# Optimization experiments

Hardware: AMD Instinct MI355X
Metric: run time of the kernel (lower is better)

The kernel has to match this reference:

```python
import jax, jax.numpy as jnp
import numpy as np

N_NODES = 50000
N_EDGES = 800000
IN_FEATS = 256
N_HEADS = 4
OUT_FEATS = 32
NEG_SLOPE = 0.2


def setup_inputs() -> dict:
    key = jax.random.key(0)
    k_feat, k_src, k_dst, k_fc, k_al, k_ar, k_res = jax.random.split(key, 7)
    feat = jax.random.normal(k_feat, (N_NODES, IN_FEATS), dtype=jnp.float32)
    src = jax.random.randint(k_src, (N_EDGES,), 0, N_NODES)
    dst = jax.random.randint(k_dst, (N_EDGES,), 0, N_NODES)
    # xavier-normal-ish scales
    s_fc = (2.0 / (IN_FEATS + N_HEADS * OUT_FEATS)) ** 0.5
    W_fc = jax.random.normal(k_fc, (N_HEADS * OUT_FEATS, IN_FEATS), dtype=jnp.float32) * s_fc
    s_a = (2.0 / (1 + N_HEADS * OUT_FEATS)) ** 0.5
    attn_l = jax.random.normal(k_al, (N_HEADS, OUT_FEATS), dtype=jnp.float32) * s_a
    attn_r = jax.random.normal(k_ar, (N_HEADS, OUT_FEATS), dtype=jnp.float32) * s_a
    W_res = jax.random.normal(k_res, (N_HEADS * OUT_FEATS, IN_FEATS), dtype=jnp.float32) * s_fc
    return {"feat": feat, "src": src, "dst": dst, "W_fc": W_fc,
            "attn_l": attn_l, "attn_r": attn_r, "W_res": W_res}


def reference(feat, src, dst, W_fc, attn_l, attn_r, W_res):
    N = feat.shape[0]
    H, D = attn_l.shape
    ones_e = jnp.ones(src.shape[0], dtype=feat.dtype)

    # projection: [N, H, D]
    h = (feat @ W_fc.T).reshape(N, H, D)
    feat_dst = h  # dst features are pre-norm (torch code aliases before * norm)

    # symmetric norm on source side: out_degree^-0.5
    out_deg = jax.ops.segment_sum(ones_e, src, num_segments=N)
    feat_src = h * (jnp.clip(out_deg, 1.0) ** -0.5)[:, None, None]

    # per-node attention halves -> per-edge score, leaky relu
    el = jnp.einsum('nhd,hd->nh', feat_src, attn_l)  # [N, H]
    er = jnp.einsum('nhd,hd->nh', feat_dst, attn_r)  # [N, H]
    e = jax.nn.leaky_relu(el[src] + er[dst], NEG_SLOPE)  # [E, H]

    # edge_softmax over incoming edges of each dst node
    emax = jax.ops.segment_max(e, dst, num_segments=N)
    emax = jnp.where(jnp.isfinite(emax), emax, 0.0)  # guard empty segments
    ex = jnp.exp(e - emax[dst])
    denom = jax.ops.segment_sum(ex, dst, num_segments=N)
    a = ex / denom[dst]  # [E, H]

    # weighted scatter-sum of messages: u_mul_e + sum
    msg = feat_src[src] * a[:, :, None]  # [E, H, D]
    rst = jax.ops.segment_sum(msg, dst, num_segments=N)  # [N, H, D]

    # symmetric norm on destination side: in_degree^0.5
    in_deg = jax.ops.segment_sum(ones_e, dst, num_segments=N)
    rst = rst * jnp.sqrt(jnp.clip(in_deg, 1.0))[:, None, None]

    # residual projection
    rst = rst + (feat @ W_res.T).reshape(N, H, D)
    return rst
```

## Files before the change

### kernel.cpp

```cpp
#include <hip/hip_runtime.h>
#include <hip/hip_bf16.h>
#include <math.h>

#define HD 128
#define IN_F 256
#define NEG_SLOPE 0.2f
#define NMAX 50000
#define GGRID 256
#define CSRC 32

typedef __attribute__((ext_vector_type(8))) short short8;
typedef __attribute__((ext_vector_type(4))) float f32x4;

__device__ __forceinline__ unsigned short f2bf(float x) {
    __hip_bfloat16 b = __float2bfloat16(x);
    return *(unsigned short*)&b;
}
__device__ __forceinline__ float bf2f(unsigned short u) {
    unsigned int v = ((unsigned int)u) << 16;
    float f;
    __builtin_memcpy(&f, &v, 4);
    return f;
}
__device__ __forceinline__ short8 pack8(float4 f0, float4 f1) {
    short8 v;
    v[0] = (short)f2bf(f0.x); v[1] = (short)f2bf(f0.y);
    v[2] = (short)f2bf(f0.z); v[3] = (short)f2bf(f0.w);
    v[4] = (short)f2bf(f1.x); v[5] = (short)f2bf(f1.y);
    v[6] = (short)f2bf(f1.z); v[7] = (short)f2bf(f1.w);
    return v;
}

__global__ __launch_bounds__(256) void cvt_ew_kernel(
    const float4* __restrict__ wfc4, const float4* __restrict__ wres4,
    const float* __restrict__ wfc, const float* __restrict__ attn_l,
    const float* __restrict__ attn_r, ushort4* __restrict__ w16,
    unsigned short* __restrict__ ew16, int n4each) {
    int b = blockIdx.x;
    if (b < 4) {
        int h = b, k = threadIdx.x;
        float sl = 0.f, sr = 0.f;
#pragma unroll 8
        for (int d = 0; d < 32; d++) {
            float w = wfc[(size_t)(h * 32 + d) * IN_F + k];
            sl += attn_l[h * 32 + d] * w;
            sr += attn_r[h * 32 + d] * w;
        }
        ew16[h * IN_F + k] = f2bf(sl);
        ew16[(4 + h) * IN_F + k] = f2bf(sr);
        ew16[(8 + h) * IN_F + k] = 0;
        ew16[(12 + h) * IN_F + k] = 0;
        return;
    }
    int idx = (b - 4) * 256 + threadIdx.x;
    if (idx >= 2 * n4each) return;
    float4 f = (idx < n4each) ? wfc4[idx] : wres4[idx - n4each];
    ushort4 u;
    u.x = f2bf(f.x); u.y = f2bf(f.y); u.z = f2bf(f.z); u.w = f2bf(f.w);
    w16[idx] = u;
}

__global__ __launch_bounds__(512) void hist_kernel(const int* __restrict__ src,
                                                   const int* __restrict__ dst,
                                                   unsigned short* __restrict__ pc_src,
                                                   unsigned short* __restrict__ pc_dst,
                                                   int N, int E, int C, int chunk,
                                                   int chunk_s) {
    __shared__ unsigned int h[NMAX / 2];
    int tid = threadIdx.x;
    int nh = N >> 1;
    uint4* h4 = (uint4*)h;
    for (int i = tid; i < (nh >> 2); i += 512) h4[i] = make_uint4(0, 0, 0, 0);
    for (int i = (nh & ~3) + tid; i < nh; i += 512) h[i] = 0;
    __syncthreads();

    int b = blockIdx.x;
    bool isSrc = (b >= C);
    const int* arr = isSrc ? src : dst;
    int c = isSrc ? (b - C) : b;
    int ch = isSrc ? chunk_s : chunk;
    int e0 = c * ch, e1 = min(E, (c + 1) * ch);
    for (int e = e0 + tid; e < e1; e += 512) {
        int v = arr[e];
        atomicAdd(&h[v >> 1], 1u << ((v & 1) << 4));
    }
    __syncthreads();

    unsigned short* pc = (isSrc ? pc_src : pc_dst) + (size_t)c * N;
    uint4* pc4 = (uint4*)pc;
    for (int i = tid; i < (nh >> 2); i += 512) pc4[i] = h4[i];
    for (int i = (nh & ~3) + tid; i < nh; i += 512) ((unsigned int*)pc)[i] = h[i];
}

__global__ __launch_bounds__(256) void sum_scan1_kernel(
    const unsigned short* __restrict__ pc_src, unsigned short* __restrict__ pc_dst,
    int* __restrict__ out_cnt, int* __restrict__ deg, int* __restrict__ bsum,
    int N, int C) {
    __shared__ int wsum[4];
    int n = blockIdx.x * 256 + threadIdx.x;
    int sd = 0;
    if (n < N) {
        int ss = 0;
#pragma unroll 4
        for (int c = 0; c < CSRC; c++) ss += pc_src[(size_t)c * N + n];
        for (int c = 0; c < C; c++) {
            unsigned short v = pc_dst[(size_t)c * N + n];
            pc_dst[(size_t)c * N + n] = (unsigned short)sd;
            sd += v;
        }
        out_cnt[n] = ss;
        deg[n] = sd;
    }
    int v = (n < N) ? sd : 0;
#pragma unroll
    for (int d = 1; d < 64; d <<= 1) v += __shfl_xor(v, d);
    if ((threadIdx.x & 63) == 0) wsum[threadIdx.x >> 6] = v;
    __syncthreads();
    if (threadIdx.x == 0) bsum[blockIdx.x] = wsum[0] + wsum[1] + wsum[2] + wsum[3];
}

__global__ __launch_bounds__(256) void scan3_kernel(const int* __restrict__ deg,
                                                    const int* __restrict__ bsum,
                                                    int* __restrict__ row_start,
                                                    int N, int nb, int E) {
    __shared__ int wsum[4];
    __shared__ int sbo[256];
    int tid = threadIdx.x, lane = tid & 63, wid = tid >> 6;
    {
        int v = (tid < nb) ? bsum[tid] : 0;
        int incl = v;
#pragma unroll
        for (int d = 1; d < 64; d <<= 1) {
            int t = __shfl_up(incl, d);
            if (lane >= d) incl += t;
        }
        if (lane == 63) wsum[wid] = incl;
        __syncthreads();
        int woff = 0;
        for (int w = 0; w < wid; w++) woff += wsum[w];
        sbo[tid] = woff + incl - v;
        __syncthreads();
    }
    int boff = sbo[blockIdx.x];
    if (blockIdx.x == 0 && tid == 0) row_start[N] = E;
    __syncthreads();

    int i = blockIdx.x * 256 + tid;
    int v = (i < N) ? deg[i] : 0;
    int incl = v;
#pragma unroll
    for (int d = 1; d < 64; d <<= 1) {
        int t = __shfl_up(incl, d);
        if (lane >= d) incl += t;
    }
    if (lane == 63) wsum[wid] = incl;
    __syncthreads();
    int woff = 0;
    for (int w = 0; w < wid; w++) woff += wsum[w];
    int excl = boff + woff + incl - v;
    if (i < N) row_start[i] = excl;
}

__global__ __launch_bounds__(512) void place_kernel(const int* __restrict__ src,
                                                    const int* __restrict__ dst,
                                                    const unsigned short* __restrict__ chunkpre,
                                                    const int* __restrict__ row_start,
                                                    int* __restrict__ esrc,
                                                    int N, int E, int chunk) {
    __shared__ unsigned int cur[NMAX / 2];
    int tid = threadIdx.x;
    int nh = N >> 1;
    const unsigned short* cp = chunkpre + (size_t)blockIdx.x * N;
    const uint4* cp4 = (const uint4*)cp;
    uint4* cur4 = (uint4*)cur;
    for (int i = tid; i < (nh >> 2); i += 512) cur4[i] = cp4[i];
    for (int i = (nh & ~3) + tid; i < nh; i += 512) cur[i] = ((const unsigned int*)cp)[i];
    __syncthreads();

    int e1 = min(E, (int)(blockIdx.x + 1) * chunk);
    for (int e = blockIdx.x * chunk + tid; e < e1; e += 512) {
        int d = dst[e], s = src[e];
        int sh = (d & 1) << 4;
        unsigned int old = atomicAdd(&cur[d >> 1], 1u << sh);
        int rank = (old >> sh) & 0xffff;
        esrc[row_start[d] + rank] = s;
    }
}

__global__ __launch_bounds__(512, 1) void gemm_fused(
    const float* __restrict__ feat, const __hip_bfloat16* __restrict__ w16,
    const __hip_bfloat16* __restrict__ ew16, const int* __restrict__ out_cnt,
    unsigned short* __restrict__ h16, unsigned short* __restrict__ resid16,
    float* __restrict__ el, float* __restrict__ er, int N, int ntiles) {
    __shared__ unsigned short sB[256 * 256];
    __shared__ unsigned short sA[32 * 256];
    int tid = threadIdx.x;
    int lane = tid & 63, w = tid >> 6;
    int l15 = lane & 15, lg = lane >> 4;
    int c0 = w * 32;
    bool w0 = (w == 0);
    bool isH = (w < 4);
    int colloc = c0 & 127;

#pragma unroll
    for (int it = 0; it < 16; ++it) {
        int idx = it * 512 + tid;
        int c = idx >> 5, g = idx & 31;
        short8 v = *(const short8*)(w16 + (size_t)c * IN_F + g * 8);
        *(short8*)&sB[c * 256 + ((g ^ (c & 7)) * 8)] = v;
    }
    short8 ereg[8];
    if (w0) {
        const __hip_bfloat16* ep = ew16 + (size_t)l15 * IN_F + lg * 8;
#pragma unroll
        for (int kk = 0; kk < 8; kk++) ereg[kk] = *(const short8*)(ep + kk * 32);
    }

    int srow[2], sgc[2];
#pragma unroll
    for (int i = 0; i < 2; i++) {
        int idx = i * 512 + tid;
        srow[i] = idx >> 5;
        sgc[i] = idx & 31;
    }

    float4 fA[2][2];
    int t = blockIdx.x;
#pragma unroll
    for (int i = 0; i < 2; i++) {
        int gm = t * 32 + srow[i];
        gm = (gm < N) ? gm : (N - 1);
        const float4* fp = (const float4*)(feat + (size_t)gm * IN_F + sgc[i] * 8);
        fA[i][0] = fp[0];
        fA[i][1] = fp[1];
    }

    for (; t < ntiles; t += GGRID) {
        __syncthreads();
#pragma unroll
        for (int i = 0; i < 2; i++)
            *(short8*)&sA[srow[i] * 256 + ((sgc[i] ^ (srow[i] & 7)) * 8)] =
                pack8(fA[i][0], fA[i][1]);
        __syncthreads();

        int tn = t + GGRID;
        if (tn < ntiles) {
#pragma unroll
            for (int i = 0; i < 2; i++) {
                int gm = tn * 32 + srow[i];
                gm = (gm < N) ? gm : (N - 1);
                const float4* fp = (const float4*)(feat + (size_t)gm * IN_F + sgc[i] * 8);
                fA[i][0] = fp[0];
                fA[i][1] = fp[1];
            }
        }

        f32x4 acc[2][2], accE[2];
#pragma unroll
        for (int i = 0; i < 2; i++) {
            accE[i] = (f32x4){0.f, 0.f, 0.f, 0.f};
#pragma unroll
            for (int j = 0; j < 2; j++) acc[i][j] = (f32x4){0.f, 0.f, 0.f, 0.f};
        }
#pragma unroll
        for (int kk = 0; kk < 8; kk++) {
            short8 a[2], b[2];
#pragma unroll
            for (int mi = 0; mi < 2; mi++) {
                int row = mi * 16 + l15;
                int gs = (kk * 4 + lg) ^ (row & 7);
                a[mi] = *(const short8*)&sA[row * 256 + gs * 8];
            }
#pragma unroll
            for (int ni = 0; ni < 2; ni++) {
                int c = c0 + ni * 16 + l15;
                int gsb = (kk * 4 + lg) ^ (c & 7);
                b[ni] = *(const short8*)&sB[c * 256 + gsb * 8];
            }
#pragma unroll
            for (int mi = 0; mi < 2; mi++)
#pragma unroll
                for (int ni = 0; ni < 2; ni++)
                    acc[mi][ni] = __builtin_amdgcn_mfma_f32_16x16x32_bf16(
                        a[mi], b[ni], acc[mi][ni], 0, 0, 0);
            if (w0) {
#pragma unroll
                for (int mi = 0; mi < 2; mi++)
                    accE[mi] = __builtin_amdgcn_mfma_f32_16x16x32_bf16(
                        a[mi], ereg[kk], accE[mi], 0, 0, 0);
            }
        }

        int bm = t * 32;
#pragma unroll
        for (int mi = 0; mi < 2; mi++) {
#pragma unroll
            for (int reg = 0; reg < 4; reg++) {
                int r = bm + mi * 16 + lg * 4 + reg;
                bool valid = (r < N);
                int rr = valid ? r : 0;
                if (isH) {
                    float nrm = rsqrtf(fmaxf((float)out_cnt[rr], 1.0f));
                    if (valid) {
#pragma unroll
                        for (int ni = 0; ni < 2; ni++)
                            h16[(size_t)r * HD + colloc + ni * 16 + l15] =
                                f2bf(acc[mi][ni][reg] * nrm);
                        if (w0) {
                            float ev = accE[mi][reg];
                            if (l15 < 4) el[r * 4 + l15] = ev * nrm;
                            else if (l15 < 8) er[r * 4 + (l15 - 4)] = ev;
                        }
                    }
                } else if (valid) {
#pragma unroll
                    for (int ni = 0; ni < 2; ni++)
                        resid16[(size_t)r * HD + colloc + ni * 16 + l15] =
                            f2bf(acc[mi][ni][reg]);
                }
            }
        }
    }
}

__global__ __launch_bounds__(256) void agg_kernel(const unsigned short* __restrict__ h16,
                                                  const float* __restrict__ el,
                                                  const float* __restrict__ er,
                                                  const int* __restrict__ row_start,
                                                  const int* __restrict__ esrc,
                                                  const unsigned short* __restrict__ resid16,
                                                  float* __restrict__ out, int N) {
    int wid = threadIdx.x >> 6, lane = threadIdx.x & 63;
    int n = blockIdx.x * 4 + wid;
    if (n >= N) return;
    int es = lane >> 4;
    int l15 = lane & 15;
    int h = l15 >> 2;
    int d0 = l15 * 8;
    int beg = row_start[n], end = row_start[n + 1];
    float erh = er[n * 4 + h];
    float den = 0.f;
    float acc[8];
#pragma unroll
    for (int j = 0; j < 8; j++) acc[j] = 0.f;

    if (beg < end) {
        bool ok[4]; float ev[4]; short8 hv[4];
        auto LOAD = [&](int base, bool* okk, float* evv, short8* hvv) {
#pragma unroll
            for (int u = 0; u < 4; u++) {
                int idx = base + u * 4 + es;
                okk[u] = idx < end;
                int s = esrc[okk[u] ? idx : beg];
                evv[u] = el[s * 4 + h];
                hvv[u] = *(const short8*)(h16 + (size_t)s * HD + d0);
            }
        };
        auto COMPUTE = [&](const bool* okk, const float* evv, const short8* hvv) {
#pragma unroll
            for (int u = 0; u < 4; u++) {
                float e = evv[u] + erh;
                e = (e > 0.f) ? e : NEG_SLOPE * e;
                float ex = okk[u] ? __expf(e) : 0.f;
                den += ex;
#pragma unroll
                for (int j = 0; j < 8; j++)
                    acc[j] += ex * bf2f((unsigned short)hvv[u][j]);
            }
        };
        LOAD(beg, ok, ev, hv);
        for (int base = beg + 16; base < end; base += 16) {
            bool ok2[4]; float ev2[4]; short8 hv2[4];
            LOAD(base, ok2, ev2, hv2);
            COMPUTE(ok, ev, hv);
#pragma unroll
            for (int u = 0; u < 4; u++) { ok[u] = ok2[u]; ev[u] = ev2[u]; hv[u] = hv2[u]; }
        }
        COMPUTE(ok, ev, hv);
    }

#pragma unroll
    for (int m = 16; m < 64; m <<= 1) {
        den += __shfl_xor(den, m);
#pragma unroll
        for (int j = 0; j < 8; j++) acc[j] += __shfl_xor(acc[j], m);
    }

    if (es == 0) {
        const unsigned short* rp = resid16 + (size_t)n * HD + d0;
        short8 rv = *(const short8*)rp;
        int indeg = end - beg;
        float sc = (indeg > 0) ? sqrtf((float)indeg) / den : 0.f;
        float o[8];
#pragma unroll
        for (int j = 0; j < 8; j++)
            o[j] = sc * acc[j] + bf2f((unsigned short)rv[j]);
        float* op = out + (size_t)n * HD + d0;
        *(float4*)op = make_float4(o[0], o[1], o[2], o[3]);
        *(float4*)(op + 4) = make_float4(o[4], o[5], o[6], o[7]);
    }
}

extern "C" void kernel_launch(void* const* d_in, const int* in_sizes, int n_in,
                              void* d_out, int out_size, void* d_ws, size_t ws_size,
                              hipStream_t stream) {
    const float* feat   = (const float*)d_in[0];
    const int*   src    = (const int*)d_in[1];
    const int*   dst    = (const int*)d_in[2];
    const float* W_fc   = (const float*)d_in[3];
    const float* attn_l = (const float*)d_in[4];
    const float* attn_r = (const float*)d_in[5];
    const float* W_res  = (const float*)d_in[6];
    float* out = (float*)d_out;

    int N = in_sizes[0] / IN_F;
    int E = in_sizes[1];
    int nb = (N + 255) / 256;

    size_t off = 0;
    auto alloc = [&](size_t bytes) {
        size_t o = off;
        off = (off + bytes + 255) & ~(size_t)255;
        return o;
    };
    char* ws = (char*)d_ws;
    unsigned short* h16     = (unsigned short*)(ws + alloc((size_t)N * HD * 2));
    unsigned short* resid16 = (unsigned short*)(ws + alloc((size_t)N * HD * 2));
    __hip_bfloat16* w16     = (__hip_bfloat16*)(ws + alloc((size_t)2 * HD * IN_F * 2));
    unsigned short* ew16    = (unsigned short*)(ws + alloc((size_t)16 * IN_F * 2));
    float* el               = (float*)(ws + alloc((size_t)N * 4 * 4));
    float* er               = (float*)(ws + alloc((size_t)N * 4 * 4));
    int* out_cnt            = (int*)(ws + alloc((size_t)N * 4));
    int* deg                = (int*)(ws + alloc((size_t)N * 4));
    int* row_start          = (int*)(ws + alloc((size_t)(N + 1) * 4));
    int* bsum               = (int*)(ws + alloc((size_t)nb * 4));
    int* esrc               = (int*)(ws + alloc((size_t)E * 4));
    unsigned short* pc_src  = (unsigned short*)(ws + alloc((size_t)CSRC * N * 2));

    size_t per_chunk = (size_t)2 * N;
    size_t avail = (ws_size > off + 4096) ? (ws_size - off - 4096) : 0;
    int C = (int)(avail / per_chunk);
    if (C > 128) C = 128;
    if (C < 32) C = 32;
    unsigned short* pc_dst = (unsigned short*)(ws + alloc((size_t)C * N * 2));
    int chunk = (E + C - 1) / C;
    int chunk_s = (E + CSRC - 1) / CSRC;

    int n4each = HD * IN_F / 4;
    int cvtb = (2 * n4each + 255) / 256;
    cvt_ew_kernel<<<4 + cvtb, 256, 0, stream>>>(
        (const float4*)W_fc, (const float4*)W_res, W_fc, attn_l, attn_r,
        (ushort4*)w16, ew16, n4each);

    hist_kernel<<<C + CSRC, 512, 0, stream>>>(src, dst, pc_src, pc_dst,
                                              N, E, C, chunk, chunk_s);
    sum_scan1_kernel<<<nb, 256, 0, stream>>>(pc_src, pc_dst, out_cnt, deg, bsum, N, C);
    scan3_kernel<<<nb, 256, 0, stream>>>(deg, bsum, row_start, N, nb, E);
    place_kernel<<<C, 512, 0, stream>>>(src, dst, pc_dst, row_start, esrc, N, E, chunk);

    int ntiles = (N + 31) / 32;
    gemm_fused<<<GGRID, 512, 0, stream>>>(feat, (const __hip_bfloat16*)w16,
                                          (const __hip_bfloat16*)ew16, out_cnt,
                                          h16, resid16, el, er, N, ntiles);

    int nb4 = (N + 3) / 4;
    agg_kernel<<<nb4, 256, 0, stream>>>(h16, el, er, row_start, esrc, resid16, out, N);
}
```

Baseline: 148.7 us.

## Double block sizes for CSR build and GEMM, shrink agg prefetch depth

The histogram and placement kernels now launch 1024 threads per block instead of 512, so each block's large LDS histogram is cleared, filled and copied by twice as many threads. The fused GEMM also moves to 1024 threads with 16 waves, each owning 16 output columns instead of 32, which halves per-wave register use and the MFMA work per wave. The aggregation kernel prefetches 2 edges per lane-group per step instead of 4. That cuts registers and raises occupancy, at the cost of less memory-level parallelism per thread on the gather.

```diff
diff --git a/kernel.cpp b/kernel.cpp
--- a/kernel.cpp
+++ b/kernel.cpp
@@ -60,18 +60,18 @@
     w16[idx] = u;
 }
 
-__global__ __launch_bounds__(512) void hist_kernel(const int* __restrict__ src,
-                                                   const int* __restrict__ dst,
-                                                   unsigned short* __restrict__ pc_src,
-                                                   unsigned short* __restrict__ pc_dst,
-                                                   int N, int E, int C, int chunk,
-                                                   int chunk_s) {
+__global__ __launch_bounds__(1024) void hist_kernel(const int* __restrict__ src,
+                                                    const int* __restrict__ dst,
+                                                    unsigned short* __restrict__ pc_src,
+                                                    unsigned short* __restrict__ pc_dst,
+                                                    int N, int E, int C, int chunk,
+                                                    int chunk_s) {
     __shared__ unsigned int h[NMAX / 2];
     int tid = threadIdx.x;
     int nh = N >> 1;
     uint4* h4 = (uint4*)h;
-    for (int i = tid; i < (nh >> 2); i += 512) h4[i] = make_uint4(0, 0, 0, 0);
-    for (int i = (nh & ~3) + tid; i < nh; i += 512) h[i] = 0;
+    for (int i = tid; i < (nh >> 2); i += 1024) h4[i] = make_uint4(0, 0, 0, 0);
+    for (int i = (nh & ~3) + tid; i < nh; i += 1024) h[i] = 0;
     __syncthreads();
 
     int b = blockIdx.x;
@@ -80,7 +80,7 @@
     int c = isSrc ? (b - C) : b;
     int ch = isSrc ? chunk_s : chunk;
     int e0 = c * ch, e1 = min(E, (c + 1) * ch);
-    for (int e = e0 + tid; e < e1; e += 512) {
+    for (int e = e0 + tid; e < e1; e += 1024) {
         int v = arr[e];
         atomicAdd(&h[v >> 1], 1u << ((v & 1) << 4));
     }
@@ -88,8 +88,8 @@
 
     unsigned short* pc = (isSrc ? pc_src : pc_dst) + (size_t)c * N;
     uint4* pc4 = (uint4*)pc;
-    for (int i = tid; i < (nh >> 2); i += 512) pc4[i] = h4[i];
-    for (int i = (nh & ~3) + tid; i < nh; i += 512) ((unsigned int*)pc)[i] = h[i];
+    for (int i = tid; i < (nh >> 2); i += 1024) pc4[i] = h4[i];
+    for (int i = (nh & ~3) + tid; i < nh; i += 1024) ((unsigned int*)pc)[i] = h[i];
 }
 
 __global__ __launch_bounds__(256) void sum_scan1_kernel(
@@ -161,24 +161,24 @@
     if (i < N) row_start[i] = excl;
 }
 
-__global__ __launch_bounds__(512) void place_kernel(const int* __restrict__ src,
-                                                    const int* __restrict__ dst,
-                                                    const unsigned short* __restrict__ chunkpre,
-                                                    const int* __restrict__ row_start,
-                                                    int* __restrict__ esrc,
-                                                    int N, int E, int chunk) {
+__global__ __launch_bounds__(1024) void place_kernel(const int* __restrict__ src,
+                                                     const int* __restrict__ dst,
+                                                     const unsigned short* __restrict__ chunkpre,
+                                                     const int* __restrict__ row_start,
+                                                     int* __restrict__ esrc,
+                                                     int N, int E, int chunk) {
     __shared__ unsigned int cur[NMAX / 2];
     int tid = threadIdx.x;
     int nh = N >> 1;
     const unsigned short* cp = chunkpre + (size_t)blockIdx.x * N;
     const uint4* cp4 = (const uint4*)cp;
     uint4* cur4 = (uint4*)cur;
-    for (int i = tid; i < (nh >> 2); i += 512) cur4[i] = cp4[i];
-    for (int i = (nh & ~3) + tid; i < nh; i += 512) cur[i] = ((const unsigned int*)cp)[i];
+    for (int i = tid; i < (nh >> 2); i += 1024) cur4[i] = cp4[i];
+    for (int i = (nh & ~3) + tid; i < nh; i += 1024) cur[i] = ((const unsigned int*)cp)[i];
     __syncthreads();
 
     int e1 = min(E, (int)(blockIdx.x + 1) * chunk);
-    for (int e = blockIdx.x * chunk + tid; e < e1; e += 512) {
+    for (int e = blockIdx.x * chunk + tid; e < e1; e += 1024) {
         int d = dst[e], s = src[e];
         int sh = (d & 1) << 4;
         unsigned int old = atomicAdd(&cur[d >> 1], 1u << sh);
@@ -187,7 +187,7 @@
     }
 }
 
-__global__ __launch_bounds__(512, 1) void gemm_fused(
+__global__ __launch_bounds__(1024, 1) void gemm_fused(
     const float* __restrict__ feat, const __hip_bfloat16* __restrict__ w16,
     const __hip_bfloat16* __restrict__ ew16, const int* __restrict__ out_cnt,
     unsigned short* __restrict__ h16, unsigned short* __restrict__ resid16,
@@ -197,14 +197,14 @@
     int tid = threadIdx.x;
     int lane = tid & 63, w = tid >> 6;
     int l15 = lane & 15, lg = lane >> 4;
-    int c0 = w * 32;
+    int c0 = w * 16;
     bool w0 = (w == 0);
-    bool isH = (w < 4);
+    bool isH = (w < 8);
     int colloc = c0 & 127;
 
 #pragma unroll
-    for (int it = 0; it < 16; ++it) {
-        int idx = it * 512 + tid;
+    for (int it = 0; it < 8; ++it) {
+        int idx = it * 1024 + tid;
         int c = idx >> 5, g = idx & 31;
         short8 v = *(const short8*)(w16 + (size_t)c * IN_F + g * 8);
         *(short8*)&sB[c * 256 + ((g ^ (c & 7)) * 8)] = v;
@@ -216,73 +216,56 @@
         for (int kk = 0; kk < 8; kk++) ereg[kk] = *(const short8*)(ep + kk * 32);
     }
 
-    int srow[2], sgc[2];
-#pragma unroll
-    for (int i = 0; i < 2; i++) {
-        int idx = i * 512 + tid;
-        srow[i] = idx >> 5;
-        sgc[i] = idx & 31;
-    }
-
-    float4 fA[2][2];
+    int srow = tid >> 5, sgc = tid & 31;
+
+    float4 fA0, fA1;
     int t = blockIdx.x;
-#pragma unroll
-    for (int i = 0; i < 2; i++) {
-        int gm = t * 32 + srow[i];
+    {
+        int gm = t * 32 + srow;
         gm = (gm < N) ? gm : (N - 1);
-        const float4* fp = (const float4*)(feat + (size_t)gm * IN_F + sgc[i] * 8);
-        fA[i][0] = fp[0];
-        fA[i][1] = fp[1];
+        const float4* fp = (const float4*)(feat + (size_t)gm * IN_F + sgc * 8);
+        fA0 = fp[0];
+        fA1 = fp[1];
     }
 
     for (; t < ntiles; t += GGRID) {
         __syncthreads();
-#pragma unroll
-        for (int i = 0; i < 2; i++)
-            *(short8*)&sA[srow[i] * 256 + ((sgc[i] ^ (srow[i] & 7)) * 8)] =
-                pack8(fA[i][0], fA[i][1]);
+        *(short8*)&sA[srow * 256 + ((sgc ^ (srow & 7)) * 8)] = pack8(fA0, fA1);
         __syncthreads();
 
         int tn = t + GGRID;
         if (tn < ntiles) {
-#pragma unroll
-            for (int i = 0; i < 2; i++) {
-                int gm = tn * 32 + srow[i];
-                gm = (gm < N) ? gm : (N - 1);
-                const float4* fp = (const float4*)(feat + (size_t)gm * IN_F + sgc[i] * 8);
-                fA[i][0] = fp[0];
-                fA[i][1] = fp[1];
-            }
-        }
-
-        f32x4 acc[2][2], accE[2];
+            int gm = tn * 32 + srow;
+            gm = (gm < N) ? gm : (N - 1);
+            const float4* fp = (const float4*)(feat + (size_t)gm * IN_F + sgc * 8);
+            fA0 = fp[0];
+            fA1 = fp[1];
+        }
+
+        f32x4 acc[2], accE[2];
 #pragma unroll
         for (int i = 0; i < 2; i++) {
+            acc[i] = (f32x4){0.f, 0.f, 0.f, 0.f};
             accE[i] = (f32x4){0.f, 0.f, 0.f, 0.f};
-#pragma unroll
-            for (int j = 0; j < 2; j++) acc[i][j] = (f32x4){0.f, 0.f, 0.f, 0.f};
         }
 #pragma unroll
         for (int kk = 0; kk < 8; kk++) {
-            short8 a[2], b[2];
+            short8 a[2], b;
 #pragma unroll
             for (int mi = 0; mi < 2; mi++) {
                 int row = mi * 16 + l15;
                 int gs = (kk * 4 + lg) ^ (row & 7);
                 a[mi] = *(const short8*)&sA[row * 256 + gs * 8];
             }
-#pragma unroll
-            for (int ni = 0; ni < 2; ni++) {
-                int c = c0 + ni * 16 + l15;
+            {
+                int c = c0 + l15;
                 int gsb = (kk * 4 + lg) ^ (c & 7);
-                b[ni] = *(const short8*)&sB[c * 256 + gsb * 8];
+                b = *(const short8*)&sB[c * 256 + gsb * 8];
             }
 #pragma unroll
             for (int mi = 0; mi < 2; mi++)
-#pragma unroll
-                for (int ni = 0; ni < 2; ni++)
-                    acc[mi][ni] = __builtin_amdgcn_mfma_f32_16x16x32_bf16(
-                        a[mi], b[ni], acc[mi][ni], 0, 0, 0);
+                acc[mi] = __builtin_amdgcn_mfma_f32_16x16x32_bf16(a[mi], b, acc[mi],
+                                                                  0, 0, 0);
             if (w0) {
 #pragma unroll
                 for (int mi = 0; mi < 2; mi++)
@@ -302,10 +285,8 @@
                 if (isH) {
                     float nrm = rsqrtf(fmaxf((float)out_cnt[rr], 1.0f));
                     if (valid) {
-#pragma unroll
-                        for (int ni = 0; ni < 2; ni++)
-                            h16[(size_t)r * HD + colloc + ni * 16 + l15] =
-                                f2bf(acc[mi][ni][reg] * nrm);
+                        h16[(size_t)r * HD + colloc + l15] =
+                            f2bf(acc[mi][reg] * nrm);
                         if (w0) {
                             float ev = accE[mi][reg];
                             if (l15 < 4) el[r * 4 + l15] = ev * nrm;
@@ -313,10 +294,7 @@
                         }
                     }
                 } else if (valid) {
-#pragma unroll
-                    for (int ni = 0; ni < 2; ni++)
-                        resid16[(size_t)r * HD + colloc + ni * 16 + l15] =
-                            f2bf(acc[mi][ni][reg]);
+                    resid16[(size_t)r * HD + colloc + l15] = f2bf(acc[mi][reg]);
                 }
             }
         }
@@ -345,38 +323,46 @@
     for (int j = 0; j < 8; j++) acc[j] = 0.f;
 
     if (beg < end) {
-        bool ok[4]; float ev[4]; short8 hv[4];
-        auto LOAD = [&](int base, bool* okk, float* evv, short8* hvv) {
-#pragma unroll
-            for (int u = 0; u < 4; u++) {
-                int idx = base + u * 4 + es;
-                okk[u] = idx < end;
-                int s = esrc[okk[u] ? idx : beg];
-                evv[u] = el[s * 4 + h];
-                hvv[u] = *(const short8*)(h16 + (size_t)s * HD + d0);
-            }
-        };
-        auto COMPUTE = [&](const bool* okk, const float* evv, const short8* hvv) {
-#pragma unroll
-            for (int u = 0; u < 4; u++) {
-                float e = evv[u] + erh;
-                e = (e > 0.f) ? e : NEG_SLOPE * e;
-                float ex = okk[u] ? __expf(e) : 0.f;
-                den += ex;
-#pragma unroll
-                for (int j = 0; j < 8; j++)
-                    acc[j] += ex * bf2f((unsigned short)hvv[u][j]);
-            }
-        };
-        LOAD(beg, ok, ev, hv);
-        for (int base = beg + 16; base < end; base += 16) {
-            bool ok2[4]; float ev2[4]; short8 hv2[4];
-            LOAD(base, ok2, ev2, hv2);
-            COMPUTE(ok, ev, hv);
-#pragma unroll
-            for (int u = 0; u < 4; u++) { ok[u] = ok2[u]; ev[u] = ev2[u]; hv[u] = hv2[u]; }
-        }
-        COMPUTE(ok, ev, hv);
+        bool ok0, ok1;
+        float ev0, ev1; short8 hv0, hv1;
+        {
+            int i0 = beg + es, i1 = beg + 4 + es;
+            ok0 = i0 < end; ok1 = i1 < end;
+            int s0 = esrc[ok0 ? i0 : beg];
+            int s1 = esrc[ok1 ? i1 : beg];
+            ev0 = el[s0 * 4 + h]; ev1 = el[s1 * 4 + h];
+            hv0 = *(const short8*)(h16 + (size_t)s0 * HD + d0);
+            hv1 = *(const short8*)(h16 + (size_t)s1 * HD + d0);
+        }
+        for (int base = beg + 8; base < end; base += 8) {
+            int i0 = base + es, i1 = base + 4 + es;
+            bool p0 = i0 < end, p1 = i1 < end;
+            int t0 = esrc[p0 ? i0 : beg];
+            int t1 = esrc[p1 ? i1 : beg];
+            float fv0 = el[t0 * 4 + h];
+            float fv1 = el[t1 * 4 + h];
+            short8 g0 = *(const short8*)(h16 + (size_t)t0 * HD + d0);
+            short8 g1 = *(const short8*)(h16 + (size_t)t1 * HD + d0);
+            float e0 = ev0 + erh; e0 = (e0 > 0.f) ? e0 : NEG_SLOPE * e0;
+            float e1 = ev1 + erh; e1 = (e1 > 0.f) ? e1 : NEG_SLOPE * e1;
+            float ex0 = ok0 ? __expf(e0) : 0.f;
+            float ex1 = ok1 ? __expf(e1) : 0.f;
+            den += ex0 + ex1;
+#pragma unroll
+            for (int j = 0; j < 8; j++)
+                acc[j] += ex0 * bf2f((unsigned short)hv0[j]) +
+                          ex1 * bf2f((unsigned short)hv1[j]);
+            ok0 = p0; ok1 = p1; ev0 = fv0; ev1 = fv1; hv0 = g0; hv1 = g1;
+        }
+        float e0 = ev0 + erh; e0 = (e0 > 0.f) ? e0 : NEG_SLOPE * e0;
+        float e1 = ev1 + erh; e1 = (e1 > 0.f) ? e1 : NEG_SLOPE * e1;
+        float ex0 = ok0 ? __expf(e0) : 0.f;
+        float ex1 = ok1 ? __expf(e1) : 0.f;
+        den += ex0 + ex1;
+#pragma unroll
+        for (int j = 0; j < 8; j++)
+            acc[j] += ex0 * bf2f((unsigned short)hv0[j]) +
+                      ex1 * bf2f((unsigned short)hv1[j]);
     }
 
 #pragma unroll
@@ -452,16 +438,16 @@
         (const float4*)W_fc, (const float4*)W_res, W_fc, attn_l, attn_r,
         (ushort4*)w16, ew16, n4each);
 
-    hist_kernel<<<C + CSRC, 512, 0, stream>>>(src, dst, pc_src, pc_dst,
-                                              N, E, C, chunk, chunk_s);
+    hist_kernel<<<C + CSRC, 1024, 0, stream>>>(src, dst, pc_src, pc_dst,
+                                               N, E, C, chunk, chunk_s);
     sum_scan1_kernel<<<nb, 256, 0, stream>>>(pc_src, pc_dst, out_cnt, deg, bsum, N, C);
     scan3_kernel<<<nb, 256, 0, stream>>>(deg, bsum, row_start, N, nb, E);
-    place_kernel<<<C, 512, 0, stream>>>(src, dst, pc_dst, row_start, esrc, N, E, chunk);
+    place_kernel<<<C, 1024, 0, stream>>>(src, dst, pc_dst, row_start, esrc, N, E, chunk);
 
     int ntiles = (N + 31) / 32;
-    gemm_fused<<<GGRID, 512, 0, stream>>>(feat, (const __hip_bfloat16*)w16,
-                                          (const __hip_bfloat16*)ew16, out_cnt,
-                                          h16, resid16, el, er, N, ntiles);
+    gemm_fused<<<GGRID, 1024, 0, stream>>>(feat, (const __hip_bfloat16*)w16,
+                                           (const __hip_bfloat16*)ew16, out_cnt,
+                                           h16, resid16, el, er, N, ntiles);
 
     int nb4 = (N + 3) / 4;
     agg_kernel<<<nb4, 256, 0, stream>>>(h16, el, er, row_start, esrc, resid16, out, N);
```

Result: faster. 141.5 us (-4.9%).
